# Optimization experiments

Hardware: AMD Instinct MI355X
Metric: run time of the kernel (lower is better)

The kernel has to match this reference:

```python
import jax, jax.numpy as jnp
import numpy as np

H_HEADS = 8
TOP_K = 32


def _interp_matrix(n_out, n_in):
    # 1D linear-interp matrix matching torch trilinear, align_corners=False
    c = (jnp.arange(n_out, dtype=jnp.float32) + 0.5) * (n_in / n_out) - 0.5
    c = jnp.clip(c, 0.0, n_in - 1)
    i0 = jnp.floor(c).astype(jnp.int32)
    i1 = jnp.minimum(i0 + 1, n_in - 1)
    w = c - i0.astype(jnp.float32)
    r = jnp.arange(n_out)
    Mt = jnp.zeros((n_out, n_in), jnp.float32)
    return Mt.at[r, i0].add(1.0 - w).at[r, i1].add(w)


def _ln(x, g, b, eps=1e-5):
    m = x.mean(axis=-1, keepdims=True)
    v = ((x - m) ** 2).mean(axis=-1, keepdims=True)
    return (x - m) * jax.lax.rsqrt(v + eps) * g + b


def _forward(x, mask, pe, Wqkv, bqkv, Wo, bo, ln1_g, ln1_b, W1, b1, W2, b2,
             ln2_g, ln2_b, gate, mem_k, mem_v, fc1_w, fc1_b, fc2_w, fc2_b):
    B, D = x.shape[0], x.shape[1]
    H, HD, K = H_HEADS, D // H_HEADS, TOP_K
    # FeatureConcatenator treated as identity (x already concatenated features)
    Im = _interp_matrix(8, mask.shape[2])  # separable trilinear resize 64->8
    m8 = jnp.einsum('ai,bj,ck,nqijk->nqabc', Im, Im, Im, mask)
    h = x * m8 + pe  # masked features + learned absolute 3D positional enc
    tok = h.reshape(B, D, -1).transpose(0, 2, 1)  # [B, S=512, D]
    scale = 1.0 / jnp.sqrt(jnp.float32(HD))
    L = Wqkv.shape[0]
    for l in range(L):
        qkv = tok @ Wqkv[l] + bqkv[l]
        q, k, v = jnp.split(qkv, 3, axis=-1)
        hd = lambda t: t.reshape(B, -1, H, HD).transpose(0, 2, 1, 3)  # [B,H,S,d]
        q, k, v = hd(q), hd(k), hd(v)
        attn = jax.nn.softmax(jnp.einsum('bhsd,bhtd->bhst', q, k) * scale, axis=-1)
        out = jnp.einsum('bhst,bhtd->bhsd', attn, v)
        if l == 0:  # KNN memory layer: irregular top-k retrieval over memory bank
            sim = jnp.einsum('bhsd,bmd->bhsm', q, mem_k) * scale  # [B,H,S,M]
            top_sim, top_idx = jax.lax.top_k(sim, K)  # [B,H,S,K]
            mv = jnp.take_along_axis(mem_v[:, None, None], top_idx[..., None], axis=3)
            mem_out = jnp.einsum('bhsk,bhskd->bhsd', jax.nn.softmax(top_sim, axis=-1), mv)
            g = jax.nn.sigmoid(gate)[None, :, None, None]
            out = out * (1.0 - g) + mem_out * g
        out = out.transpose(0, 2, 1, 3).reshape(B, -1, D)
        tok = _ln(tok + out @ Wo[l] + bo[l], ln1_g[l], ln1_b[l])
        ff = jax.nn.gelu(tok @ W1[l] + b1[l], approximate=False) @ W2[l] + b2[l]
        tok = _ln(tok + ff, ln2_g[l], ln2_b[l])
    pooled = tok.mean(axis=1)  # global avg pool over all 512 voxels
    return jax.nn.gelu(pooled @ fc1_w + fc1_b, approximate=False) @ fc2_w + fc2_b


def setup_inputs() -> dict:
    key = jax.random.key(0)
    ks = jax.random.split(key, 24)
    B, D, Sp, M, L = 4, 512, 8, 8192, 6
    H, HD, FF, MLP, NC = 8, 64, 2048, 1024, 117
    nrm = lambda k, shp, s=0.02: jax.random.normal(k, shp, jnp.float32) * s
    return {
        'x': jax.random.normal(ks[0], (B, D, Sp, Sp, Sp), jnp.float32),
        'mask': jax.random.uniform(ks[1], (B, 1, 64, 64, 64), jnp.float32),
        'pe': nrm(ks[2], (1, D, Sp, Sp, Sp)),
        'Wqkv': nrm(ks[3], (L, D, 3 * D)),
        'bqkv': jnp.zeros((L, 3 * D), jnp.float32),
        'Wo': nrm(ks[4], (L, D, D)),
        'bo': jnp.zeros((L, D), jnp.float32),
        'ln1_g': jnp.ones((L, D), jnp.float32),
        'ln1_b': jnp.zeros((L, D), jnp.float32),
        'W1': nrm(ks[5], (L, D, FF)),
        'b1': jnp.zeros((L, FF), jnp.float32),
        'W2': nrm(ks[6], (L, FF, D)),
        'b2': jnp.zeros((L, D), jnp.float32),
        'ln2_g': jnp.ones((L, D), jnp.float32),
        'ln2_b': jnp.zeros((L, D), jnp.float32),
        'gate': jnp.zeros((H,), jnp.float32),
        'mem_k': jax.random.normal(ks[7], (B, M, HD), jnp.float32),
        'mem_v': jax.random.normal(ks[8], (B, M, HD), jnp.float32),
        'fc1_w': nrm(ks[9], (D, MLP)),
        'fc1_b': jnp.zeros((MLP,), jnp.float32),
        'fc2_w': nrm(ks[10], (MLP, NC)),
        'fc2_b': jnp.zeros((NC,), jnp.float32),
    }


def reference(x, mask, pe, Wqkv, bqkv, Wo, bo, ln1_g, ln1_b, W1, b1, W2, b2,
              ln2_g, ln2_b, gate, mem_k, mem_v, fc1_w, fc1_b, fc2_w, fc2_b):
    return _forward(x, mask, pe, Wqkv, bqkv, Wo, bo, ln1_g, ln1_b, W1, b1, W2,
                    b2, ln2_g, ln2_b, gate, mem_k, mem_v, fc1_w, fc1_b, fc2_w, fc2_b)
```

## Files before the change

kernel.cpp:

```cpp
#include <hip/hip_runtime.h>
#include <hip/hip_bf16.h>
#include <float.h>
#include <math.h>

#define NB 4
#define ND 512
#define NS 512
#define NH 8
#define NHD 64
#define NM 8192
#define NL 6
#define NFF 2048
#define NMLP 1024
#define NC 117

#define KCC 64
#define NCC (NM / KCC)
#define CAPB 160
#define TRIG 96

#define CAPS 352
#define TRIGS 96

#define AS1 __attribute__((address_space(1)))
// ... 6 lines not shown
    return 0.5f * x * (1.0f + erff(x * 0.70710678118654752440f));
}

__device__ __forceinline__ ushort f2bf_rne(float x) {
    uint u = __float_as_uint(x);
    uint r = u + 0x7FFFu + ((u >> 16) & 1u);
    return (ushort)(r >> 16);
}
__device__ __forceinline__ float bf2f(ushort h) { return __uint_as_float(((uint)h) << 16); }
__device__ __forceinline__ void split1(float x, ushort& h, ushort& l) {
    h = f2bf_rne(x);
    float r = x - bf2f(h);
    l = f2bf_rne(r);
}
__device__ __forceinline__ void split8(const float* v, s16x8& hv, s16x8& lv) {
#pragma unroll
    for (int j = 0; j < 8; ++j) {
        ushort h, l;
        split1(v[j], h, l);
        hv[j] = (short)h;
        lv[j] = (short)l;
    }
}

__device__ __forceinline__ unsigned long long packkey(float v, int idx) {
    uint u = __float_as_uint(v);
    u = u ^ (((int)u < 0) ? 0xFFFFFFFFu : 0x80000000u);
    return (((unsigned long long)u) << 13) | (unsigned long long)(8191 - idx);
}
__device__ __forceinline__ float keyval(unsigned long long K) {
    uint vb = (uint)(K >> 13);
    uint orig = (vb & 0x80000000u) ? (vb ^ 0x80000000u) : ~vb;
    return __uint_as_float(orig);
}

__device__ __forceinline__ void shrink_cheap(float* __restrict__ cval,
                                             ushort* __restrict__ cidx,
                                             int q, int n, int lane,
                                             float* __restrict__ thrOut) {
    if (n < 32) return;
    int j0 = lane, j1 = lane + 64, j2 = lane + 128;
    bool o0 = j0 < n, o1 = j1 < n, o2 = j2 < n;
    float v0 = o0 ? cval[q * CAPB + j0] : 0.f;
    float v1 = o1 ? cval[q * CAPB + j1] : 0.f;
    float v2 = o2 ? cval[q * CAPB + j2] : 0.f;
    ushort i0 = o0 ? cidx[q * CAPB + j0] : 0;
    ushort i1 = o1 ? cidx[q * CAPB + j1] : 0;
    ushort i2 = o2 ? cidx[q * CAPB + j2] : 0;
    unsigned long long k0 = o0 ? packkey(v0, (int)i0) : 0ULL;
    unsigned long long k1 = o1 ? packkey(v1, (int)i1) : 0ULL;
    unsigned long long k2 = o2 ? packkey(v2, (int)i2) : 0ULL;
    unsigned long long lo = 0, hi = (1ULL << 45) - 1;
    while (lo < hi) {
        unsigned long long mid = (lo + hi + 1) >> 1;
        int c = (int)__popcll(__ballot(k0 >= mid)) + (int)__popcll(__ballot(k1 >= mid)) +
                (int)__popcll(__ballot(k2 >= mid));
        if (c >= 32) lo = mid;
        else hi = mid - 1;
    }
    unsigned long long K = lo;
    unsigned long long lm = (1ULL << lane) - 1;
    int base = 0;
    {
        unsigned long long m = __ballot(k0 >= K);
        if (k0 >= K) { int p = base + (int)__popcll(m & lm); cval[q * CAPB + p] = v0; cidx[q * CAPB + p] = i0; }
        base += (int)__popcll(m);
    }
    {
        unsigned long long m = __ballot(k1 >= K);
        if (k1 >= K) { int p = base + (int)__popcll(m & lm); cval[q * CAPB + p] = v1; cidx[q * CAPB + p] = i1; }
        base += (int)__popcll(m);
    }
    {
        unsigned long long m = __ballot(k2 >= K);
        if (k2 >= K) { int p = base + (int)__popcll(m & lm); cval[q * CAPB + p] = v2; cidx[q * CAPB + p] = i2; }
        base += (int)__popcll(m);
    }
    if (thrOut && lane == 0) *thrOut = keyval(K);
}

__device__ __forceinline__ float shrink6b(float* __restrict__ bv,
                                          ushort* __restrict__ bi,
                                          int n, int lane) {
    int j0 = lane, j1 = lane + 64, j2 = lane + 128, j3 = lane + 192, j4 = lane + 256, j5 = lane + 320;
    bool o0 = j0 < n, o1 = j1 < n, o2 = j2 < n, o3 = j3 < n, o4 = j4 < n, o5 = j5 < n;
    float v0 = o0 ? bv[j0] : 0.f, v1 = o1 ? bv[j1] : 0.f, v2 = o2 ? bv[j2] : 0.f;
    float v3 = o3 ? bv[j3] : 0.f, v4 = o4 ? bv[j4] : 0.f, v5 = o5 ? bv[j5] : 0.f;
    ushort i0 = o0 ? bi[j0] : 0, i1 = o1 ? bi[j1] : 0, i2 = o2 ? bi[j2] : 0;
    ushort i3 = o3 ? bi[j3] : 0, i4 = o4 ? bi[j4] : 0, i5 = o5 ? bi[j5] : 0;
    unsigned long long k0 = o0 ? packkey(v0, (int)i0) : 0ULL;
    unsigned long long k1 = o1 ? packkey(v1, (int)i1) : 0ULL;
    unsigned long long k2 = o2 ? packkey(v2, (int)i2) : 0ULL;
    unsigned long long k3 = o3 ? packkey(v3, (int)i3) : 0ULL;
    unsigned long long k4 = o4 ? packkey(v4, (int)i4) : 0ULL;
    unsigned long long k5 = o5 ? packkey(v5, (int)i5) : 0ULL;
    unsigned long long lo = 0, hi = (1ULL << 45) - 1;
    while (lo < hi) {
        unsigned long long mid = (lo + hi + 1) >> 1;
        int c = (int)__popcll(__ballot(k0 >= mid)) + (int)__popcll(__ballot(k1 >= mid)) +
                (int)__popcll(__ballot(k2 >= mid)) + (int)__popcll(__ballot(k3 >= mid)) +
                (int)__popcll(__ballot(k4 >= mid)) + (int)__popcll(__ballot(k5 >= mid));
        if (c >= 32) lo = mid;
        else hi = mid - 1;
    }
    unsigned long long K = lo;
    unsigned long long lm = (1ULL << lane) - 1;
    int base = 0;
    {
        unsigned long long m = __ballot(k0 >= K);
        if (k0 >= K) { int p = base + (int)__popcll(m & lm); bv[p] = v0; bi[p] = i0; }
        base += (int)__popcll(m);
    }
    {
        unsigned long long m = __ballot(k1 >= K);
        if (k1 >= K) { int p = base + (int)__popcll(m & lm); bv[p] = v1; bi[p] = i1; }
        base += (int)__popcll(m);
    }
    {
        unsigned long long m = __ballot(k2 >= K);
        if (k2 >= K) { int p = base + (int)__popcll(m & lm); bv[p] = v2; bi[p] = i2; }
        base += (int)__popcll(m);
    }
    {
        unsigned long long m = __ballot(k3 >= K);
        if (k3 >= K) { int p = base + (int)__popcll(m & lm); bv[p] = v3; bi[p] = i3; }
        base += (int)__popcll(m);
    }
    {
        unsigned long long m = __ballot(k4 >= K);
        if (k4 >= K) { int p = base + (int)__popcll(m & lm); bv[p] = v4; bi[p] = i4; }
        base += (int)__popcll(m);
    }
    {
        unsigned long long m = __ballot(k5 >= K);
        if (k5 >= K) { int p = base + (int)__popcll(m & lm); bv[p] = v5; bi[p] = i5; }
        base += (int)__popcll(m);
    }
    return keyval(K);
}
// ... 132 lines not shown
        int k = ty * 8 + i;
        t[tx][k] = Wl[(size_t)(k0 + k) * N + n0 + tx];
    }
    __syncthreads();
    int tid = ty * 32 + tx;
    int r = tid >> 3, gg = tid & 7;
    float v[8];
#pragma unroll
    for (int j = 0; j < 8; ++j) v[j] = t[r][gg * 8 + j];
    s16x8 hv, lv;
    split8(v, hv, lv);
    size_t byte = (size_t)(n0 + r) * (2 * K) + (size_t)(k0 >> 6) * 128 +
                  (size_t)(((gg * 16)) ^ ((r & 7) << 4));
    *(s16x8*)((char*)WHl + byte) = hv;
    *(s16x8*)((char*)WLl + byte) = lv;
}

__global__ void k_asplit(const float* __restrict__ X, ushort* __restrict__ XH,
                         ushort* __restrict__ XL, int K) {
    int id = blockIdx.x * 256 + threadIdx.x;
    int gtot = K >> 3;
    int m = id / gtot, g = id - m * gtot;
    const float* src = X + (size_t)m * K + g * 8;
    float v[8];
    *(float4*)&v[0] = *(const float4*)(src);
    *(float4*)&v[4] = *(const float4*)(src + 4);
    s16x8 hv, lv;
    split8(v, hv, lv);
    int kc = g >> 3, gg = g & 7;
    size_t byte = (size_t)m * (2 * K) + (size_t)kc * 128 +
                  (size_t)((gg * 16) ^ ((m & 7) << 4));
    *(s16x8*)((char*)XH + byte) = hv;
    *(s16x8*)((char*)XL + byte) = lv;
}

__global__ void k_qkvsplit(const float* __restrict__ qkv, ushort* __restrict__ QH,
                           ushort* __restrict__ QL, ushort* __restrict__ KH,
                           ushort* __restrict__ KL) {
    int id = blockIdx.x * 256 + threadIdx.x;
    int r = id >> 3, g = id & 7;
    int b = r >> 12, h = (r >> 9) & 7, s = r & 511;
    const float* base = qkv + ((size_t)(b * NS + s)) * 1536 + h * 64 + g * 8;
    size_t byte = (size_t)r * 128 + (size_t)((g * 16) ^ ((r & 7) << 4));
    float v[8];
#pragma unroll
    for (int j = 0; j < 8; ++j) v[j] = base[j] * 0.125f;
    s16x8 hv, lv;
    split8(v, hv, lv);
    *(s16x8*)((char*)QH + byte) = hv;
    *(s16x8*)((char*)QL + byte) = lv;
#pragma unroll
    for (int j = 0; j < 8; ++j) v[j] = base[512 + j];
    split8(v, hv, lv);
    *(s16x8*)((char*)KH + byte) = hv;
    *(s16x8*)((char*)KL + byte) = lv;
}

__global__ __launch_bounds__(256) void k_vsplitT(const float* __restrict__ qkv,
                                                 ushort* __restrict__ VTH,
                                                 ushort* __restrict__ VTL) {
    __shared__ float t[64][65];
    int sb = blockIdx.x, h = blockIdx.y, b = blockIdx.z;
    int tid = threadIdx.x;
    {
        int sl = tid >> 2, dseg = (tid & 3) * 16;
        const float* src = qkv + ((size_t)(b * NS) + sb * 64 + sl) * 1536 + 1024 + h * 64 + dseg;
#pragma unroll
        for (int i = 0; i < 4; ++i) {
            float4 v = *(const float4*)(src + i * 4);
            t[sl][dseg + i * 4 + 0] = v.x;
            t[sl][dseg + i * 4 + 1] = v.y;
            t[sl][dseg + i * 4 + 2] = v.z;
            t[sl][dseg + i * 4 + 3] = v.w;
        }
    }
    __syncthreads();
    {
        int dr = tid >> 2, sseg = (tid & 3) * 16;
        size_t rb = ((size_t)(b * NH + h) * 64 + dr) * 1024 + (size_t)sb * 128;
        char* oh = (char*)VTH + rb;
        char* ol = (char*)VTL + rb;
        int sw = (dr & 7) << 4;
#pragma unroll
        for (int i = 0; i < 16; ++i) {
            int s = sseg + i;
            float v = t[s][dr];
            ushort hh, ll;
            split1(v, hh, ll);
            int by = (((s >> 3) * 16) ^ sw) + (s & 7) * 2;
            *(ushort*)(oh + by) = hh;
            *(ushort*)(ol + by) = ll;
        }
    }
}

template <int BM, int BN, int EPI>
__global__ __launch_bounds__(256) void k_gmm(
    const float* __restrict__ A, const float* __restrict__ W,
    const float* __restrict__ bias, const float* __restrict__ resid,
    float* __restrict__ C, int M, int N, int K) {
    constexpr int PAD = 40;
    constexpr int FM = BM / 32, FN = BN / 32;
    __shared__ __align__(16) ushort Ah[BM * PAD];
    __shared__ __align__(16) ushort Al[BM * PAD];
    __shared__ __align__(16) ushort Bh[BN * PAD];
    __shared__ __align__(16) ushort Bl[BN * PAD];
    int tid = threadIdx.x, lane = tid & 63, wvi = tid >> 6;
    int wr = wvi >> 1, wc = wvi & 1;
    int bn = blockIdx.x * BN, bm = blockIdx.y * BM;
    constexpr int FPTA = BM / 8;
    constexpr int TPRA = 32 / FPTA;
    int arow = tid / TPRA;
    int akoff = (tid % TPRA) * FPTA;
    const float* Ap = A + (size_t)(bm + arow) * K + akoff;
    constexpr int FPTB = BN / 8;
    int bkrow = tid >> 3;
    int bnoff = (tid & 7) * FPTB;
    const float* Wp = W + (size_t)bkrow * N + bn + bnoff;
    float abuf[FPTA], bbuf[FPTB];
#pragma unroll
    for (int j = 0; j < FPTA; j += 4) *(float4*)&abuf[j] = *(const float4*)(Ap + j);
#pragma unroll
    for (int j = 0; j < FPTB; j += 4) *(float4*)&bbuf[j] = *(const float4*)(Wp + j);
    f32x4 acc[FM][FN] = {};
    for (int k0 = 0; k0 < K; k0 += 32) {
#pragma unroll
// ... 38 lines not shown
#pragma unroll
            for (int fn = 0; fn < FN; ++fn) {
                acc[fm][fn] = __builtin_amdgcn_mfma_f32_16x16x32_bf16(fah[fm], fbh[fn], acc[fm][fn], 0, 0, 0);
                acc[fm][fn] = __builtin_amdgcn_mfma_f32_16x16x32_bf16(fah[fm], fbl[fn], acc[fm][fn], 0, 0, 0);
                acc[fm][fn] = __builtin_amdgcn_mfma_f32_16x16x32_bf16(fal[fm], fbh[fn], acc[fm][fn], 0, 0, 0);
            }
        __syncthreads();
    }
#pragma unroll
    for (int fm = 0; fm < FM; ++fm) {
#pragma unroll
        for (int fn = 0; fn < FN; ++fn) {
            int n = bn + wc * (BN / 2) + fn * 16 + (lane & 15);
            float bb = 0.f;
            if (EPI != 3) bb = bias[n];
#pragma unroll
            for (int r = 0; r < 4; ++r) {
                int m = bm + wr * (BM / 2) + fm * 16 + (lane >> 4) * 4 + r;
                float o = acc[fm][fn][r] + bb;
                if (EPI == 1) o = gelu_f(o);
                else if (EPI == 2) o += resid[(size_t)m * N + n];
                C[(size_t)m * N + n] = o;
            }
        }
    }
}

template <int BM, int BN, int EPI>
__global__ __launch_bounds__(256) void k_gmm2(
    const ushort* __restrict__ AH, const ushort* __restrict__ AL,
    const ushort* __restrict__ BH, const ushort* __restrict__ BL,
    const float* __restrict__ bias, const float* __restrict__ resid,
    float* __restrict__ C, ushort* __restrict__ CH, ushort* __restrict__ CL,
    int M, int N, int K) {
    constexpr int FM = BM / 32, FN = BN / 32;
    __shared__ __align__(16) ushort sAh[BM * 64];
    __shared__ __align__(16) ushort sAl[BM * 64];
    __shared__ __align__(16) ushort sBh[BN * 64];
    __shared__ __align__(16) ushort sBl[BN * 64];
    int tid = threadIdx.x, lane = tid & 63, wvi = tid >> 6;
    int wr = wvi >> 1, wc = wvi & 1;
    int bn = blockIdx.x * BN, bm = blockIdx.y * BM;
    int rloc = tid >> 3, bgr = (tid & 7) * 16;
    size_t rowstride = (size_t)(2 * K);
    f32x4 acc[FM][FN] = {};

    for (int k0 = 0; k0 < K; k0 += 64) {
        __syncthreads();
        size_t kcb = (size_t)k0 * 2;
#pragma unroll
        for (int i = 0; i < BM / 32; ++i) {
            int r = i * 32 + rloc;
            size_t g = (size_t)(bm + r) * rowstride + kcb + bgr;
            __builtin_amdgcn_global_load_lds((const AS1 uint*)((const char*)AH + g),
                                             (AS3 uint*)((char*)sAh + r * 128 + bgr), 16, 0, 0);
            __builtin_amdgcn_global_load_lds((const AS1 uint*)((const char*)AL + g),
                                             (AS3 uint*)((char*)sAl + r * 128 + bgr), 16, 0, 0);
        }
#pragma unroll
        for (int i = 0; i < BN / 32; ++i) {
            int r = i * 32 + rloc;
            size_t g = (size_t)(bn + r) * rowstride + kcb + bgr;
            __builtin_amdgcn_global_load_lds((const AS1 uint*)((const char*)BH + g),
                                             (AS3 uint*)((char*)sBh + r * 128 + bgr), 16, 0, 0);
            __builtin_amdgcn_global_load_lds((const AS1 uint*)((const char*)BL + g),
                                             (AS3 uint*)((char*)sBl + r * 128 + bgr), 16, 0, 0);
// ... 16 lines not shown
                int by = row * 128 + (kbyte ^ ((row & 7) << 4));
                fbh[fn] = *(const s16x8*)((const char*)sBh + by);
                fbl[fn] = *(const s16x8*)((const char*)sBl + by);
            }
#pragma unroll
            for (int fm = 0; fm < FM; ++fm)
#pragma unroll
                for (int fn = 0; fn < FN; ++fn) {
                    acc[fm][fn] = __builtin_amdgcn_mfma_f32_16x16x32_bf16(fah[fm], fbh[fn], acc[fm][fn], 0, 0, 0);
                    acc[fm][fn] = __builtin_amdgcn_mfma_f32_16x16x32_bf16(fah[fm], fbl[fn], acc[fm][fn], 0, 0, 0);
                    acc[fm][fn] = __builtin_amdgcn_mfma_f32_16x16x32_bf16(fal[fm], fbh[fn], acc[fm][fn], 0, 0, 0);
                }
        }
    }
#pragma unroll
    for (int fm = 0; fm < FM; ++fm) {
#pragma unroll
        for (int fn = 0; fn < FN; ++fn) {
            int n = bn + wc * (BN / 2) + fn * 16 + (lane & 15);
            float bb = 0.f;
            if (EPI != 3) bb = bias[n];
#pragma unroll
            for (int r = 0; r < 4; ++r) {
                int m = bm + wr * (BM / 2) + fm * 16 + (lane >> 4) * 4 + r;
                float o = acc[fm][fn][r] + bb;
                if (EPI == 4) {
                    o = gelu_f(o);
                    ushort hh, ll;
                    split1(o, hh, ll);
                    size_t byb = (size_t)m * 2 * N + (size_t)(n >> 6) * 128 +
                                 (size_t)(((((n >> 3) & 7) * 16)) ^ ((m & 7) << 4)) + (n & 7) * 2;
                    *(ushort*)((char*)CH + byb) = hh;
                    *(ushort*)((char*)CL + byb) = ll;
                } else {
                    if (EPI == 1) o = gelu_f(o);
                    else if (EPI == 2) o += resid[(size_t)m * N + n];
                    C[(size_t)m * N + n] = o;
                }
            }
        }
    }
}

__global__ __launch_bounds__(256) void k_attn2(
    const ushort* __restrict__ QH, const ushort* __restrict__ QL,
    const ushort* __restrict__ KH, const ushort* __restrict__ KL,
    const ushort* __restrict__ VTH, const ushort* __restrict__ VTL,
    float* __restrict__ ao) {
    __shared__ __align__(16) char SM[81920];
    int qt = blockIdx.x, h = blockIdx.y, b = blockIdx.z;
    int tid = threadIdx.x, lane = tid & 63, wvi = tid >> 6;
    size_t R = ((size_t)(b * NH + h)) * NS;
    const char* KHg = (const char*)KH + R * 128;
    const char* KLg = (const char*)KL + R * 128;
    const char* VHg = (const char*)VTH + ((size_t)(b * NH + h) * 64) * 1024;
    const char* VLg = (const char*)VTL + ((size_t)(b * NH + h) * 64) * 1024;

    stage_lin((const char*)QH + (R + qt * 64) * 128, SM + 65536, wvi, lane);
    stage_lin((const char*)QL + (R + qt * 64) * 128, SM + 73728, wvi, lane);
    stage_lin(KHg, SM + 0, wvi, lane);
    stage_lin(KLg, SM + 8192, wvi, lane);
    stage_vt(VHg, 0, SM + 32768, wvi, lane);
    stage_vt(VLg, 0, SM + 40960, wvi, lane);
    __syncthreads();

    s16x8 fqh[2], fql[2];
// ... 188 lines not shown
            int idx = tid + i * 256;
            int r = idx >> 6, d = idx & 63;
            ks[r][d] = base[(size_t)(c * 64 + r) * 1536 + 1024 + h * 64 + d];
        }
        __syncthreads();
#pragma unroll 8
        for (int kk = 0; kk < 64; ++kk) {
            float p0 = sc[ty][kk], p1 = sc[ty + 16][kk];
            float v0 = ks[kk][tx], v1 = ks[kk][tx + 16], v2 = ks[kk][tx + 32], v3 = ks[kk][tx + 48];
            accp[0][0] += p0 * v0; accp[0][1] += p0 * v1; accp[0][2] += p0 * v2; accp[0][3] += p0 * v3;
            accp[1][0] += p1 * v0; accp[1][1] += p1 * v1; accp[1][2] += p1 * v2; accp[1][3] += p1 * v3;
        }
    }
    __syncthreads();
    float inv0 = 1.0f / Srow[ty], inv1 = 1.0f / Srow[ty + 16];
    size_t o0 = ((size_t)(b * NS) + s0 + ty) * ND + h * 64;
    size_t o1 = ((size_t)(b * NS) + s0 + ty + 16) * ND + h * 64;
    ao[o0 + tx] = accp[0][0] * inv0;
    ao[o0 + tx + 16] = accp[0][1] * inv0;
    ao[o0 + tx + 32] = accp[0][2] * inv0;
    ao[o0 + tx + 48] = accp[0][3] * inv0;
    ao[o1 + tx] = accp[1][0] * inv1;
    ao[o1 + tx + 16] = accp[1][1] * inv1;
    ao[o1 + tx + 32] = accp[1][2] * inv1;
    ao[o1 + tx + 48] = accp[1][3] * inv1;
}

__global__ __launch_bounds__(256) void k_ksel(
    const float* __restrict__ sims, const float* __restrict__ mv,
    const float* __restrict__ gate, float* __restrict__ ao, int b) {
    __shared__ float bval[4][CAPS];
    __shared__ ushort bidx[4][CAPS];
    int tid = threadIdx.x, lane = tid & 63, wvi = tid >> 6;
    int q = blockIdx.x * 4 + wvi;
    const float* srow = sims + (size_t)q * NM;
    float* bv = &bval[wvi][0];
    ushort* bi = &bidx[wvi][0];
    unsigned long long lm = (1ULL << lane) - 1;
    {
        float4 v = *(const float4*)(srow + lane * 4);
        int m0 = lane * 4;
        bv[m0 + 0] = v.x; bi[m0 + 0] = (ushort)(m0 + 0);
        bv[m0 + 1] = v.y; bi[m0 + 1] = (ushort)(m0 + 1);
        bv[m0 + 2] = v.z; bi[m0 + 2] = (ushort)(m0 + 2);
        bv[m0 + 3] = v.w; bi[m0 + 3] = (ushort)(m0 + 3);
    }
    float thr = shrink6b(bv, bi, 256, lane);
    int cnt = 32;
    float4 vcur = *(const float4*)(srow + 256 + lane * 4);
    for (int i = 1; i < 32; ++i) {
        float4 vnext;
        if (i + 1 < 32) vnext = *(const float4*)(srow + (size_t)(i + 1) * 256 + lane * 4);
        int m0 = i * 256 + lane * 4;
        bool px = vcur.x >= thr, py = vcur.y >= thr, pz = vcur.z >= thr, pw = vcur.w >= thr;
        unsigned long long bx = __ballot(px), by = __ballot(py), bz = __ballot(pz), bw = __ballot(pw);
        int nx = (int)__popcll(bx), ny = (int)__popcll(by), nz = (int)__popcll(bz), nw = (int)__popcll(bw);
        int b0 = cnt, b1 = b0 + nx, b2 = b1 + ny, b3 = b2 + nz;
        if (px) { int p = b0 + (int)__popcll(bx & lm); bv[p] = vcur.x; bi[p] = (ushort)(m0 + 0); }
        if (py) { int p = b1 + (int)__popcll(by & lm); bv[p] = vcur.y; bi[p] = (ushort)(m0 + 1); }
        if (pz) { int p = b2 + (int)__popcll(bz & lm); bv[p] = vcur.z; bi[p] = (ushort)(m0 + 2); }
        if (pw) { int p = b3 + (int)__popcll(bw & lm); bv[p] = vcur.w; bi[p] = (ushort)(m0 + 3); }
        cnt = b3 + nw;
        if (cnt >= TRIGS) {
            thr = shrink6b(bv, bi, cnt, lane);
            cnt = 32;
        }
        vcur = vnext;
    }
    thr = shrink6b(bv, bi, cnt, lane);
    float val = (lane < 32) ? bv[lane] : -FLT_MAX;
    float mx = val;
#pragma unroll
    for (int off = 32; off; off >>= 1) mx = fmaxf(mx, __shfl_xor(mx, off));
    float e = (lane < 32) ? __expf(val - mx) : 0.f;
    float ssum = e;
#pragma unroll
    for (int off = 32; off; off >>= 1) ssum += __shfl_xor(ssum, off);
    float w = e / ssum;
    if (lane < 32) bv[lane] = w;
    float acc = 0.f;
    const float* vb = mv + (size_t)b * NM * NHD;
#pragma unroll 4
    for (int j = 0; j < 32; ++j) {
        float ww = bv[j];
        int idx = (int)bi[j];
        acc += ww * vb[(size_t)idx * NHD + lane];
    }
    int h = q >> 9, s = q & 511;
    float g = 1.0f / (1.0f + __expf(-gate[h]));
    float* aop = ao + ((size_t)(b * NS) + s) * ND + h * 64 + lane;
    *aop = *aop * (1.0f - g) + acc * g;
}

__global__ __launch_bounds__(256, 2) void k_knn5(
    const float* __restrict__ qkv, const ushort* __restrict__ mkh,
    const ushort* __restrict__ mkl, const float* __restrict__ mv,
    const float* __restrict__ gate, float* __restrict__ ao) {
    __shared__ __align__(16) char SM[63760];
    ushort* kh0 = (ushort*)SM;
    ushort* kl0 = (ushort*)(SM + 8192);
    ushort* kh1 = (ushort*)(SM + 16384);
    ushort* kl1 = (ushort*)(SM + 24576);
    float* cval = (float*)(SM + 32768);
    ushort* cidx = (ushort*)(SM + 53248);
    float* thrV = (float*)(SM + 63488);
    int* cnt = (int*)(SM + 63616);
    int* sflag = (int*)(SM + 63744);
    ushort* qh = (ushort*)(SM + 32768);
    ushort* ql = (ushort*)(SM + 36864);
    int b = blockIdx.y, s0 = blockIdx.x * 4;
    int tid = threadIdx.x, lane = tid & 63, wvi = tid >> 6;
    const ushort* mhb = mkh + (size_t)b * NM * 64;
    const ushort* mlb = mkl + (size_t)b * NM * 64;
    {
        int q = tid >> 3, dbase = (tid & 7) * 8;
        const float* src = &qkv[((size_t)(b * NS) + s0 + (q & 3)) * 1536 + (q >> 2) * 64 + dbase];
        float v[8];
#pragma unroll
        for (int j = 0; j < 8; ++j) v[j] = src[j] * 0.125f;
        s16x8 hv, lv;
        split8(v, hv, lv);
        int by = q * 128 + ((dbase * 2) ^ ((q & 7) << 4));
        *(s16x8*)((char*)qh + by) = hv;
        *(s16x8*)((char*)ql + by) = lv;
// ... 231 lines not shown
    const float* b2   = (const float*)d_in[12];
    const float* ln2g = (const float*)d_in[13];
    const float* ln2b = (const float*)d_in[14];
    const float* gate = (const float*)d_in[15];
    const float* memk = (const float*)d_in[16];
    const float* memv = (const float*)d_in[17];
    const float* fc1w = (const float*)d_in[18];
    const float* fc1b = (const float*)d_in[19];
    const float* fc2w = (const float*)d_in[20];
    const float* fc2b = (const float*)d_in[21];
    float* out = (float*)d_out;

    float* ws = (float*)d_ws;

    float* m8     = ws;
    ushort* mkh   = (ushort*)(m8 + 2048);
    ushort* mkl   = mkh + 2097152;
    float* tok    = (float*)(mkl + 2097152);
    float* qkv    = tok + 1048576;
    float* ao     = qkv + 3145728;
    float* pooled = ao + 1048576;
    float* o1     = pooled + 2048;
    ushort* aH    = (ushort*)(o1 + 4096);
    ushort* aL    = aH + 1048576;
    ushort* WqTH  = aL + 1048576;
    ushort* WqTL  = WqTH + 4718592;
    ushort* WoTH  = WqTL + 4718592;
    ushort* WoTL  = WoTH + 1572864;
    ushort* W1TH  = WoTL + 1572864;
    ushort* W1TL  = W1TH + 6291456;
    ushort* W2TH  = W1TL + 6291456;
    ushort* W2TL  = W2TH + 6291456;
    float* simsb  = (float*)(W2TL + 6291456);
    float* ff1  = simsb;
    ushort* fH  = (ushort*)(simsb + 4194304);
    ushort* fL  = fH + 4194304;
    float* ybuf = simsb + 8388608;
    ushort* KHb  = (ushort*)(simsb + 9437184);
    ushort* KLb  = KHb + 1048576;
    ushort* VTHb = KLb + 1048576;
    ushort* VTLb = VTHb + 1048576;
    (void)ff1;

    size_t needNew = (size_t)((simsb + 33554432) - ws) * sizeof(float);

    if (ws_size >= needNew) {
        k_m8<<<NB, 512, 0, stream>>>(mask, m8);
        k_mksplit<<<1024, 256, 0, stream>>>(memk, mkh, mkl);
        k_tok<<<dim3(16, 16, NB), dim3(32, 8), 0, stream>>>(x, pe, m8, tok);
        k_wsplitT<<<dim3(48, 8, 6), dim3(32, 8), 0, stream>>>(Wqkv, WqTH, WqTL, 512, 1536);
        k_wsplitT<<<dim3(16, 8, 6), dim3(32, 8), 0, stream>>>(Wo, WoTH, WoTL, 512, 512);
        k_wsplitT<<<dim3(64, 8, 6), dim3(32, 8), 0, stream>>>(W1, W1TH, W1TL, 512, 2048);
        k_wsplitT<<<dim3(16, 32, 6), dim3(32, 8), 0, stream>>>(W2, W2TH, W2TL, 2048, 512);
        k_asplit<<<512, 256, 0, stream>>>(tok, aH, aL, 512);

        for (int l = 0; l < NL; ++l) {
            k_gmm2<128, 128, 0><<<dim3(12, 16), 256, 0, stream>>>(
                aH, aL, WqTH + (size_t)l * 786432, WqTL + (size_t)l * 786432,
                bqkv + l * 1536, nullptr, qkv, nullptr, nullptr, 2048, 1536, 512);
            k_qkvsplit<<<512, 256, 0, stream>>>(qkv, aH, aL, KHb, KLb);
            k_vsplitT<<<dim3(8, NH, NB), 256, 0, stream>>>(qkv, VTHb, VTLb);
            k_attn2<<<dim3(8, NH, NB), 256, 0, stream>>>(aH, aL, KHb, KLb, VTHb, VTLb, ao);
            if (l == 0) {
                for (int bb = 0; bb < NB; ++bb) {
                    k_gmm2<128, 128, 3><<<dim3(64, 32), 256, 0, stream>>>(
                        aH + (size_t)bb * 262144, aL + (size_t)bb * 262144,
                        mkh + (size_t)bb * 524288, mkl + (size_t)bb * 524288,
                        nullptr, nullptr, simsb, nullptr, nullptr, 4096, 8192, 64);
                    k_ksel<<<1024, 256, 0, stream>>>(simsb, memv, gate, ao, bb);
                }
            }
            k_asplit<<<512, 256, 0, stream>>>(ao, aH, aL, 512);
            k_gmm2<64, 64, 2><<<dim3(8, 32), 256, 0, stream>>>(
                aH, aL, WoTH + (size_t)l * 262144, WoTL + (size_t)l * 262144,
                bo + l * 512, tok, ybuf, nullptr, nullptr, 2048, 512, 512);
            k_ln2<<<2048, 256, 0, stream>>>(ybuf, ln1g + l * 512, ln1b + l * 512, tok, aH, aL);
            k_gmm2<128, 128, 4><<<dim3(16, 16), 256, 0, stream>>>(
                aH, aL, W1TH + (size_t)l * 1048576, W1TL + (size_t)l * 1048576,
                b1 + l * 2048, nullptr, nullptr, fH, fL, 2048, 2048, 512);
            k_gmm2<64, 64, 2><<<dim3(8, 32), 256, 0, stream>>>(
                fH, fL, W2TH + (size_t)l * 1048576, W2TL + (size_t)l * 1048576,
                b2 + l * 512, tok, ybuf, nullptr, nullptr, 2048, 512, 2048);
            k_ln2<<<2048, 256, 0, stream>>>(ybuf, ln2g + l * 512, ln2b + l * 512, tok, aH, aL);
        }
        k_pool<<<NB, 512, 0, stream>>>(tok, pooled);
        k_fc1<<<16, 256, 0, stream>>>(pooled, fc1w, fc1b, o1);
        k_fc2<<<2, 256, 0, stream>>>(o1, fc2w, fc2b, out);
        return;
    }

    float* m8b     = ws;
    ushort* mkh2   = (ushort*)(m8b + 2048);
    ushort* mkl2   = mkh2 + 2097152;
    float* tok2    = (float*)(mkl2 + 2097152);
    float* qkv2    = tok2 + 1048576;
    float* ao2     = qkv2 + 3145728;
    float* ybuf2   = ao2 + 1048576;
    float* ff12    = ybuf2 + 1048576;
    float* pooled2 = ff12 + 4194304;
    float* o12     = pooled2 + 2048;
    float* qmat2   = o12 + 4096;
    float* memkT2  = qmat2 + 1048576;
    float* simsb2  = memkT2 + 2097152;

    size_t needMid = (size_t)((simsb2 + 33554432) - ws) * sizeof(float);
    bool big = ws_size >= needMid;

    k_m8<<<NB, 512, 0, stream>>>(mask, m8b);
    if (big)
        k_memkT<<<dim3(NM / 32, 2, NB), dim3(32, 8), 0, stream>>>(memk, memkT2);
    else
        k_mksplit<<<1024, 256, 0, stream>>>(memk, mkh2, mkl2);
    k_tok<<<dim3(16, 16, NB), dim3(32, 8), 0, stream>>>(x, pe, m8b, tok2);

    for (int l = 0; l < NL; ++l) {
        k_gmm<128, 128, 0><<<dim3(12, 16), 256, 0, stream>>>(
            tok2, Wqkv + (size_t)l * 512 * 1536, bqkv + l * 1536, nullptr, qkv2, 2048, 1536, 512);
        k_attn<<<dim3(16, NH, NB), 256, 0, stream>>>(qkv2, ao2);
        if (l == 0) {
            if (big) {
                k_qmat<<<1024, 256, 0, stream>>>(qkv2, qmat2);
                for (int bb = 0; bb < NB; ++bb) {
                    k_gmm<128, 128, 3><<<dim3(64, 32), 256, 0, stream>>>(
                        qmat2 + (size_t)bb * 262144, memkT2 + (size_t)bb * 524288,
                        nullptr, nullptr, simsb2, 4096, 8192, 64);
                    k_ksel<<<1024, 256, 0, stream>>>(simsb2, memv, gate, ao2, bb);
                }
            } else {
                k_knn5<<<dim3(NS / 4, NB), 256, 0, stream>>>(qkv2, mkh2, mkl2, memv, gate, ao2);
            }
        }
        k_gmm<64, 64, 2><<<dim3(8, 32), 256, 0, stream>>>(
            ao2, Wo + (size_t)l * 512 * 512, bo + l * 512, tok2, ybuf2, 2048, 512, 512);
        k_ln<<<2048, 256, 0, stream>>>(ybuf2, ln1g + l * 512, ln1b + l * 512, tok2);
        k_gmm<128, 128, 1><<<dim3(16, 16), 256, 0, stream>>>(
            tok2, W1 + (size_t)l * 512 * 2048, b1 + l * 2048, nullptr, ff12, 2048, 2048, 512);
        k_gmm<64, 64, 2><<<dim3(8, 32), 256, 0, stream>>>(
            ff12, W2 + (size_t)l * 2048 * 512, b2 + l * 512, tok2, ybuf2, 2048, 512, 2048);
        k_ln<<<2048, 256, 0, stream>>>(ybuf2, ln2g + l * 512, ln2b + l * 512, tok2);
    }
    k_pool<<<NB, 512, 0, stream>>>(tok2, pooled2);
    k_fc1<<<16, 256, 0, stream>>>(pooled2, fc1w, fc1b, o12);
    k_fc2<<<2, 256, 0, stream>>>(o12, fc2w, fc2b, out);
}
```

Before: 1.435 ms.

## Fuse QKV split into GEMM epilogue and parallelize top-k selection across half-rows

The QKV GEMM now writes the hi/lo bf16-split Q (pre-scaled), K and transposed V directly in the swizzled layouts attention expects, which removes the separate qkvsplit and vsplitT kernels and the fp32 qkv round trip. The top-k selection kernel now splits each similarity row across two wavefronts that each scan half the memory bank, then merges the two candidate sets, so twice as many blocks are launched. The threshold search becomes a 32-bit radix bit search on the value with a tie fallback to the 45-bit packed key. The GEMM epilogue now uses scattered 2-byte stores, and the merge adds a block barrier.

```diff
diff --git a/kernel.cpp b/kernel.cpp
--- a/kernel.cpp
+++ b/kernel.cpp
@@ -62,6 +62,14 @@
     uint vb = (uint)(K >> 13);
     uint orig = (vb & 0x80000000u) ? (vb ^ 0x80000000u) : ~vb;
     return __uint_as_float(orig);
+}
+__device__ __forceinline__ uint sortable32(float v) {
+    uint u = __float_as_uint(v);
+    return u ^ (((int)u < 0) ? 0xFFFFFFFFu : 0x80000000u);
+}
+__device__ __forceinline__ float unsortable32(uint s) {
+    uint u = (s & 0x80000000u) ? (s ^ 0x80000000u) : ~s;
+    return __uint_as_float(u);
 }
 
 __device__ __forceinline__ void shrink_cheap(float* __restrict__ cval,
@@ -109,7 +117,7 @@
     if (thrOut && lane == 0) *thrOut = keyval(K);
 }
 
-__device__ __forceinline__ float shrink6b(float* __restrict__ bv,
+__device__ __forceinline__ float shrink6v(float* __restrict__ bv,
                                           ushort* __restrict__ bi,
                                           int n, int lane) {
     int j0 = lane, j1 = lane + 64, j2 = lane + 128, j3 = lane + 192, j4 = lane + 256, j5 = lane + 320;
@@ -118,23 +126,58 @@
     float v3 = o3 ? bv[j3] : 0.f, v4 = o4 ? bv[j4] : 0.f, v5 = o5 ? bv[j5] : 0.f;
     ushort i0 = o0 ? bi[j0] : 0, i1 = o1 ? bi[j1] : 0, i2 = o2 ? bi[j2] : 0;
     ushort i3 = o3 ? bi[j3] : 0, i4 = o4 ? bi[j4] : 0, i5 = o5 ? bi[j5] : 0;
+    uint s0 = o0 ? sortable32(v0) : 0u, s1 = o1 ? sortable32(v1) : 0u;
+    uint s2 = o2 ? sortable32(v2) : 0u, s3 = o3 ? sortable32(v3) : 0u;
+    uint s4 = o4 ? sortable32(v4) : 0u, s5 = o5 ? sortable32(v5) : 0u;
+    uint S = 0;
+#pragma unroll 1
+    for (int bit = 31; bit >= 0; --bit) {
+        uint cand = S | (1u << bit);
+        int c = (int)__popcll(__ballot(s0 >= cand)) + (int)__popcll(__ballot(s1 >= cand)) +
+                (int)__popcll(__ballot(s2 >= cand)) + (int)__popcll(__ballot(s3 >= cand)) +
+                (int)__popcll(__ballot(s4 >= cand)) + (int)__popcll(__ballot(s5 >= cand));
+        if (c >= 32) S = cand;
+    }
+    unsigned long long g0 = __ballot(s0 > S), g1 = __ballot(s1 > S), g2 = __ballot(s2 > S);
+    unsigned long long g3 = __ballot(s3 > S), g4 = __ballot(s4 > S), g5 = __ballot(s5 > S);
+    unsigned long long e0 = __ballot(o0 && s0 == S), e1 = __ballot(o1 && s1 == S), e2 = __ballot(o2 && s2 == S);
+    unsigned long long e3 = __ballot(o3 && s3 == S), e4 = __ballot(o4 && s4 == S), e5 = __ballot(o5 && s5 == S);
+    int cgt = (int)__popcll(g0) + (int)__popcll(g1) + (int)__popcll(g2) +
+              (int)__popcll(g3) + (int)__popcll(g4) + (int)__popcll(g5);
+    int ceq = (int)__popcll(e0) + (int)__popcll(e1) + (int)__popcll(e2) +
+              (int)__popcll(e3) + (int)__popcll(e4) + (int)__popcll(e5);
+    unsigned long long lm = (1ULL << lane) - 1;
+    if (cgt + ceq == 32) {
+        int base = 0;
+        if (s0 > S) { int p = base + (int)__popcll(g0 & lm); bv[p] = v0; bi[p] = i0; } base += (int)__popcll(g0);
+        if (s1 > S) { int p = base + (int)__popcll(g1 & lm); bv[p] = v1; bi[p] = i1; } base += (int)__popcll(g1);
+        if (s2 > S) { int p = base + (int)__popcll(g2 & lm); bv[p] = v2; bi[p] = i2; } base += (int)__popcll(g2);
+        if (s3 > S) { int p = base + (int)__popcll(g3 & lm); bv[p] = v3; bi[p] = i3; } base += (int)__popcll(g3);
+        if (s4 > S) { int p = base + (int)__popcll(g4 & lm); bv[p] = v4; bi[p] = i4; } base += (int)__popcll(g4);
+        if (s5 > S) { int p = base + (int)__popcll(g5 & lm); bv[p] = v5; bi[p] = i5; } base += (int)__popcll(g5);
+        if (o0 && s0 == S) { int p = base + (int)__popcll(e0 & lm); bv[p] = v0; bi[p] = i0; } base += (int)__popcll(e0);
+        if (o1 && s1 == S) { int p = base + (int)__popcll(e1 & lm); bv[p] = v1; bi[p] = i1; } base += (int)__popcll(e1);
+        if (o2 && s2 == S) { int p = base + (int)__popcll(e2 & lm); bv[p] = v2; bi[p] = i2; } base += (int)__popcll(e2);
+        if (o3 && s3 == S) { int p = base + (int)__popcll(e3 & lm); bv[p] = v3; bi[p] = i3; } base += (int)__popcll(e3);
+        if (o4 && s4 == S) { int p = base + (int)__popcll(e4 & lm); bv[p] = v4; bi[p] = i4; } base += (int)__popcll(e4);
+        if (o5 && s5 == S) { int p = base + (int)__popcll(e5 & lm); bv[p] = v5; bi[p] = i5; }
+        return unsortable32(S);
+    }
     unsigned long long k0 = o0 ? packkey(v0, (int)i0) : 0ULL;
     unsigned long long k1 = o1 ? packkey(v1, (int)i1) : 0ULL;
     unsigned long long k2 = o2 ? packkey(v2, (int)i2) : 0ULL;
     unsigned long long k3 = o3 ? packkey(v3, (int)i3) : 0ULL;
     unsigned long long k4 = o4 ? packkey(v4, (int)i4) : 0ULL;
     unsigned long long k5 = o5 ? packkey(v5, (int)i5) : 0ULL;
-    unsigned long long lo = 0, hi = (1ULL << 45) - 1;
-    while (lo < hi) {
-        unsigned long long mid = (lo + hi + 1) >> 1;
-        int c = (int)__popcll(__ballot(k0 >= mid)) + (int)__popcll(__ballot(k1 >= mid)) +
-                (int)__popcll(__ballot(k2 >= mid)) + (int)__popcll(__ballot(k3 >= mid)) +
-                (int)__popcll(__ballot(k4 >= mid)) + (int)__popcll(__ballot(k5 >= mid));
-        if (c >= 32) lo = mid;
-        else hi = mid - 1;
-    }
-    unsigned long long K = lo;
-    unsigned long long lm = (1ULL << lane) - 1;
+    unsigned long long K = 0;
+#pragma unroll 1
+    for (int bit = 44; bit >= 0; --bit) {
+        unsigned long long cand = K | (1ULL << bit);
+        int c = (int)__popcll(__ballot(k0 >= cand)) + (int)__popcll(__ballot(k1 >= cand)) +
+                (int)__popcll(__ballot(k2 >= cand)) + (int)__popcll(__ballot(k3 >= cand)) +
+                (int)__popcll(__ballot(k4 >= cand)) + (int)__popcll(__ballot(k5 >= cand));
+        if (c >= 32) K = cand;
+    }
     int base = 0;
     {
         unsigned long long m = __ballot(k0 >= K);
@@ -333,66 +376,6 @@
                   (size_t)((gg * 16) ^ ((m & 7) << 4));
     *(s16x8*)((char*)XH + byte) = hv;
     *(s16x8*)((char*)XL + byte) = lv;
-}
-
-__global__ void k_qkvsplit(const float* __restrict__ qkv, ushort* __restrict__ QH,
-                           ushort* __restrict__ QL, ushort* __restrict__ KH,
-                           ushort* __restrict__ KL) {
-    int id = blockIdx.x * 256 + threadIdx.x;
-    int r = id >> 3, g = id & 7;
-    int b = r >> 12, h = (r >> 9) & 7, s = r & 511;
-    const float* base = qkv + ((size_t)(b * NS + s)) * 1536 + h * 64 + g * 8;
-    size_t byte = (size_t)r * 128 + (size_t)((g * 16) ^ ((r & 7) << 4));
-    float v[8];
-#pragma unroll
-    for (int j = 0; j < 8; ++j) v[j] = base[j] * 0.125f;
-    s16x8 hv, lv;
-    split8(v, hv, lv);
-    *(s16x8*)((char*)QH + byte) = hv;
-    *(s16x8*)((char*)QL + byte) = lv;
-#pragma unroll
-    for (int j = 0; j < 8; ++j) v[j] = base[512 + j];
-    split8(v, hv, lv);
-    *(s16x8*)((char*)KH + byte) = hv;
-    *(s16x8*)((char*)KL + byte) = lv;
-}
-
-__global__ __launch_bounds__(256) void k_vsplitT(const float* __restrict__ qkv,
-                                                 ushort* __restrict__ VTH,
-                                                 ushort* __restrict__ VTL) {
-    __shared__ float t[64][65];
-    int sb = blockIdx.x, h = blockIdx.y, b = blockIdx.z;
-    int tid = threadIdx.x;
-    {
-        int sl = tid >> 2, dseg = (tid & 3) * 16;
-        const float* src = qkv + ((size_t)(b * NS) + sb * 64 + sl) * 1536 + 1024 + h * 64 + dseg;
-#pragma unroll
-        for (int i = 0; i < 4; ++i) {
-            float4 v = *(const float4*)(src + i * 4);
-            t[sl][dseg + i * 4 + 0] = v.x;
-            t[sl][dseg + i * 4 + 1] = v.y;
-            t[sl][dseg + i * 4 + 2] = v.z;
-            t[sl][dseg + i * 4 + 3] = v.w;
-        }
-    }
-    __syncthreads();
-    {
-        int dr = tid >> 2, sseg = (tid & 3) * 16;
-        size_t rb = ((size_t)(b * NH + h) * 64 + dr) * 1024 + (size_t)sb * 128;
-        char* oh = (char*)VTH + rb;
-        char* ol = (char*)VTL + rb;
-        int sw = (dr & 7) << 4;
-#pragma unroll
-        for (int i = 0; i < 16; ++i) {
-            int s = sseg + i;
-            float v = t[s][dr];
-            ushort hh, ll;
-            split1(v, hh, ll);
-            int by = (((s >> 3) * 16) ^ sw) + (s & 7) * 2;
-            *(ushort*)(oh + by) = hh;
-            *(ushort*)(ol + by) = ll;
-        }
-    }
 }
 
 template <int BM, int BN, int EPI>
@@ -497,6 +480,8 @@
     const ushort* __restrict__ BH, const ushort* __restrict__ BL,
     const float* __restrict__ bias, const float* __restrict__ resid,
     float* __restrict__ C, ushort* __restrict__ CH, ushort* __restrict__ CL,
+    ushort* __restrict__ C2H, ushort* __restrict__ C2L,
+    ushort* __restrict__ C3H, ushort* __restrict__ C3L,
     int M, int N, int K) {
     constexpr int FM = BM / 32, FN = BN / 32;
     __shared__ __align__(16) ushort sAh[BM * 64];
@@ -579,6 +564,31 @@
                                  (size_t)(((((n >> 3) & 7) * 16)) ^ ((m & 7) << 4)) + (n & 7) * 2;
                     *(ushort*)((char*)CH + byb) = hh;
                     *(ushort*)((char*)CL + byb) = ll;
+                } else if (EPI == 5) {
+                    int seg = n >> 9;
+                    int hh_ = (n >> 6) & 7, dd = n & 63;
+                    int bq = m >> 9, sq = m & 511;
+                    ushort hh, ll;
+                    if (seg == 0) {
+                        split1(o * 0.125f, hh, ll);
+                        size_t rr = (size_t)bq * 4096 + hh_ * 512 + sq;
+                        size_t by = rr * 128 + (size_t)((((dd >> 3) * 16)) ^ ((sq & 7) << 4)) + (dd & 7) * 2;
+                        *(ushort*)((char*)CH + by) = hh;
+                        *(ushort*)((char*)CL + by) = ll;
+                    } else if (seg == 1) {
+                        split1(o, hh, ll);
+                        size_t rr = (size_t)bq * 4096 + hh_ * 512 + sq;
+                        size_t by = rr * 128 + (size_t)((((dd >> 3) * 16)) ^ ((sq & 7) << 4)) + (dd & 7) * 2;
+                        *(ushort*)((char*)C2H + by) = hh;
+                        *(ushort*)((char*)C2L + by) = ll;
+                    } else {
+                        split1(o, hh, ll);
+                        size_t rr = (size_t)(bq * 8 + hh_) * 64 + dd;
+                        size_t by = rr * 1024 + (size_t)(sq >> 6) * 128 +
+                                    (size_t)(((((sq >> 3) & 7) * 16)) ^ ((dd & 7) << 4)) + (sq & 7) * 2;
+                        *(ushort*)((char*)C3H + by) = hh;
+                        *(ushort*)((char*)C3L + by) = ll;
+                    }
                 } else {
                     if (EPI == 1) o = gelu_f(o);
                     else if (EPI == 2) o += resid[(size_t)m * N + n];
@@ -833,64 +843,91 @@
     __shared__ float bval[4][CAPS];
     __shared__ ushort bidx[4][CAPS];
     int tid = threadIdx.x, lane = tid & 63, wvi = tid >> 6;
-    int q = blockIdx.x * 4 + wvi;
-    const float* srow = sims + (size_t)q * NM;
+    int q = blockIdx.x * 2 + (wvi >> 1);
+    int hf = wvi & 1;
+    const float* sr = sims + (size_t)q * NM + hf * 4096;
     float* bv = &bval[wvi][0];
     ushort* bi = &bidx[wvi][0];
     unsigned long long lm = (1ULL << lane) - 1;
+
     {
-        float4 v = *(const float4*)(srow + lane * 4);
+        float4 v = *(const float4*)(sr + lane * 4);
         int m0 = lane * 4;
-        bv[m0 + 0] = v.x; bi[m0 + 0] = (ushort)(m0 + 0);
-        bv[m0 + 1] = v.y; bi[m0 + 1] = (ushort)(m0 + 1);
-        bv[m0 + 2] = v.z; bi[m0 + 2] = (ushort)(m0 + 2);
-        bv[m0 + 3] = v.w; bi[m0 + 3] = (ushort)(m0 + 3);
-    }
-    float thr = shrink6b(bv, bi, 256, lane);
+        int gI = hf * 4096 + m0;
+        bv[m0 + 0] = v.x; bi[m0 + 0] = (ushort)(gI + 0);
+        bv[m0 + 1] = v.y; bi[m0 + 1] = (ushort)(gI + 1);
+        bv[m0 + 2] = v.z; bi[m0 + 2] = (ushort)(gI + 2);
+        bv[m0 + 3] = v.w; bi[m0 + 3] = (ushort)(gI + 3);
+    }
+    float thr = shrink6v(bv, bi, 256, lane);
     int cnt = 32;
-    float4 vcur = *(const float4*)(srow + 256 + lane * 4);
-    for (int i = 1; i < 32; ++i) {
-        float4 vnext;
-        if (i + 1 < 32) vnext = *(const float4*)(srow + (size_t)(i + 1) * 256 + lane * 4);
-        int m0 = i * 256 + lane * 4;
-        bool px = vcur.x >= thr, py = vcur.y >= thr, pz = vcur.z >= thr, pw = vcur.w >= thr;
+
+    float4 vA = *(const float4*)(sr + 256 + lane * 4);
+    float4 vB = *(const float4*)(sr + 512 + lane * 4);
+    for (int i = 1; i < 16; ++i) {
+        float4 vC = vB;
+        if (i + 2 < 16) vC = *(const float4*)(sr + (size_t)(i + 2) * 256 + lane * 4);
+        int m0 = hf * 4096 + i * 256 + lane * 4;
+        bool px = vA.x >= thr, py = vA.y >= thr, pz = vA.z >= thr, pw = vA.w >= thr;
         unsigned long long bx = __ballot(px), by = __ballot(py), bz = __ballot(pz), bw = __ballot(pw);
         int nx = (int)__popcll(bx), ny = (int)__popcll(by), nz = (int)__popcll(bz), nw = (int)__popcll(bw);
         int b0 = cnt, b1 = b0 + nx, b2 = b1 + ny, b3 = b2 + nz;
-        if (px) { int p = b0 + (int)__popcll(bx & lm); bv[p] = vcur.x; bi[p] = (ushort)(m0 + 0); }
-        if (py) { int p = b1 + (int)__popcll(by & lm); bv[p] = vcur.y; bi[p] = (ushort)(m0 + 1); }
-        if (pz) { int p = b2 + (int)__popcll(bz & lm); bv[p] = vcur.z; bi[p] = (ushort)(m0 + 2); }
-        if (pw) { int p = b3 + (int)__popcll(bw & lm); bv[p] = vcur.w; bi[p] = (ushort)(m0 + 3); }
+        if (px) { int p = b0 + (int)__popcll(bx & lm); bv[p] = vA.x; bi[p] = (ushort)(m0 + 0); }
+        if (py) { int p = b1 + (int)__popcll(by & lm); bv[p] = vA.y; bi[p] = (ushort)(m0 + 1); }
+        if (pz) { int p = b2 + (int)__popcll(bz & lm); bv[p] = vA.z; bi[p] = (ushort)(m0 + 2); }
+        if (pw) { int p = b3 + (int)__popcll(bw & lm); bv[p] = vA.w; bi[p] = (ushort)(m0 + 3); }
         cnt = b3 + nw;
         if (cnt >= TRIGS) {
-            thr = shrink6b(bv, bi, cnt, lane);
+            thr = shrink6v(bv, bi, cnt, lane);
             cnt = 32;
         }
-        vcur = vnext;
-    }
-    thr = shrink6b(bv, bi, cnt, lane);
-    float val = (lane < 32) ? bv[lane] : -FLT_MAX;
-    float mx = val;
-#pragma unroll
-    for (int off = 32; off; off >>= 1) mx = fmaxf(mx, __shfl_xor(mx, off));
-    float e = (lane < 32) ? __expf(val - mx) : 0.f;
-    float ssum = e;
-#pragma unroll
-    for (int off = 32; off; off >>= 1) ssum += __shfl_xor(ssum, off);
-    float w = e / ssum;
-    if (lane < 32) bv[lane] = w;
-    float acc = 0.f;
-    const float* vb = mv + (size_t)b * NM * NHD;
+        vA = vB;
+        vB = vC;
+    }
+    thr = shrink6v(bv, bi, cnt, lane);
+    __syncthreads();
+
+    if (hf == 0) {
+        float mval;
+        ushort midx;
+        if (lane < 32) { mval = bval[wvi][lane]; midx = bidx[wvi][lane]; }
+        else { mval = bval[wvi + 1][lane - 32]; midx = bidx[wvi + 1][lane - 32]; }
+        unsigned long long k = packkey(mval, (int)midx);
+        unsigned long long K = 0;
+#pragma unroll 1
+        for (int bit = 44; bit >= 0; --bit) {
+            unsigned long long cand = K | (1ULL << bit);
+            if ((int)__popcll(__ballot(k >= cand)) >= 32) K = cand;
+        }
+        unsigned long long m = __ballot(k >= K);
+        if (k >= K) {
+            int p = (int)__popcll(m & lm);
+            bv[p] = mval;
+            bi[p] = midx;
+        }
+        float val = (lane < 32) ? bv[lane] : -FLT_MAX;
+        float mx = val;
+#pragma unroll
+        for (int off = 32; off; off >>= 1) mx = fmaxf(mx, __shfl_xor(mx, off));
+        float e = (lane < 32) ? __expf(val - mx) : 0.f;
+        float ssum = e;
+#pragma unroll
+        for (int off = 32; off; off >>= 1) ssum += __shfl_xor(ssum, off);
+        float w = e / ssum;
+        if (lane < 32) bv[lane] = w;
+        float acc = 0.f;
+        const float* vb = mv + (size_t)b * NM * NHD;
 #pragma unroll 4
-    for (int j = 0; j < 32; ++j) {
-        float ww = bv[j];
-        int idx = (int)bi[j];
-        acc += ww * vb[(size_t)idx * NHD + lane];
-    }
-    int h = q >> 9, s = q & 511;
-    float g = 1.0f / (1.0f + __expf(-gate[h]));
-    float* aop = ao + ((size_t)(b * NS) + s) * ND + h * 64 + lane;
-    *aop = *aop * (1.0f - g) + acc * g;
+        for (int j = 0; j < 32; ++j) {
+            float ww = bv[j];
+            int idx = (int)bi[j];
+            acc += ww * vb[(size_t)idx * NHD + lane];
+        }
+        int h = q >> 9, s = q & 511;
+        float g = 1.0f / (1.0f + __expf(-gate[h]));
+        float* aop = ao + ((size_t)(b * NS) + s) * ND + h * 64 + lane;
+        *aop = *aop * (1.0f - g) + acc * g;
+    }
 }
 
 __global__ __launch_bounds__(256, 2) void k_knn5(
@@ -1188,15 +1225,15 @@
     ushort* W2TH  = W1TL + 6291456;
     ushort* W2TL  = W2TH + 6291456;
     float* simsb  = (float*)(W2TL + 6291456);
-    float* ff1  = simsb;
     ushort* fH  = (ushort*)(simsb + 4194304);
     ushort* fL  = fH + 4194304;
     float* ybuf = simsb + 8388608;
-    ushort* KHb  = (ushort*)(simsb + 9437184);
+    ushort* QHb  = (ushort*)qkv;
+    ushort* QLb  = QHb + 1048576;
+    ushort* KHb  = QLb + 1048576;
     ushort* KLb  = KHb + 1048576;
     ushort* VTHb = KLb + 1048576;
     ushort* VTLb = VTHb + 1048576;
-    (void)ff1;
 
     size_t needNew = (size_t)((simsb + 33554432) - ws) * sizeof(float);
 
@@ -1211,32 +1248,35 @@
         k_asplit<<<512, 256, 0, stream>>>(tok, aH, aL, 512);
 
         for (int l = 0; l < NL; ++l) {
-            k_gmm2<128, 128, 0><<<dim3(12, 16), 256, 0, stream>>>(
+            k_gmm2<128, 128, 5><<<dim3(12, 16), 256, 0, stream>>>(
                 aH, aL, WqTH + (size_t)l * 786432, WqTL + (size_t)l * 786432,
-                bqkv + l * 1536, nullptr, qkv, nullptr, nullptr, 2048, 1536, 512);
-            k_qkvsplit<<<512, 256, 0, stream>>>(qkv, aH, aL, KHb, KLb);
-            k_vsplitT<<<dim3(8, NH, NB), 256, 0, stream>>>(qkv, VTHb, VTLb);
-            k_attn2<<<dim3(8, NH, NB), 256, 0, stream>>>(aH, aL, KHb, KLb, VTHb, VTLb, ao);
+                bqkv + l * 1536, nullptr, nullptr, QHb, QLb, KHb, KLb, VTHb, VTLb,
+                2048, 1536, 512);
+            k_attn2<<<dim3(8, NH, NB), 256, 0, stream>>>(QHb, QLb, KHb, KLb, VTHb, VTLb, ao);
             if (l == 0) {
                 for (int bb = 0; bb < NB; ++bb) {
                     k_gmm2<128, 128, 3><<<dim3(64, 32), 256, 0, stream>>>(
-                        aH + (size_t)bb * 262144, aL + (size_t)bb * 262144,
+                        QHb + (size_t)bb * 262144, QLb + (size_t)bb * 262144,
                         mkh + (size_t)bb * 524288, mkl + (size_t)bb * 524288,
-                        nullptr, nullptr, simsb, nullptr, nullptr, 4096, 8192, 64);
-                    k_ksel<<<1024, 256, 0, stream>>>(simsb, memv, gate, ao, bb);
+                        nullptr, nullptr, simsb, nullptr, nullptr, nullptr, nullptr,
+                        nullptr, nullptr, 4096, 8192, 64);
+                    k_ksel<<<2048, 256, 0, stream>>>(simsb, memv, gate, ao, bb);
                 }
             }
             k_asplit<<<512, 256, 0, stream>>>(ao, aH, aL, 512);
             k_gmm2<64, 64, 2><<<dim3(8, 32), 256, 0, stream>>>(
                 aH, aL, WoTH + (size_t)l * 262144, WoTL + (size_t)l * 262144,
-                bo + l * 512, tok, ybuf, nullptr, nullptr, 2048, 512, 512);
+                bo + l * 512, tok, ybuf, nullptr, nullptr, nullptr, nullptr,
+                nullptr, nullptr, 2048, 512, 512);
             k_ln2<<<2048, 256, 0, stream>>>(ybuf, ln1g + l * 512, ln1b + l * 512, tok, aH, aL);
             k_gmm2<128, 128, 4><<<dim3(16, 16), 256, 0, stream>>>(
                 aH, aL, W1TH + (size_t)l * 1048576, W1TL + (size_t)l * 1048576,
-                b1 + l * 2048, nullptr, nullptr, fH, fL, 2048, 2048, 512);
+                b1 + l * 2048, nullptr, nullptr, fH, fL, nullptr, nullptr,
+                nullptr, nullptr, 2048, 2048, 512);
             k_gmm2<64, 64, 2><<<dim3(8, 32), 256, 0, stream>>>(
                 fH, fL, W2TH + (size_t)l * 1048576, W2TL + (size_t)l * 1048576,
-                b2 + l * 512, tok, ybuf, nullptr, nullptr, 2048, 512, 2048);
+                b2 + l * 512, tok, ybuf, nullptr, nullptr, nullptr, nullptr,
+                nullptr, nullptr, 2048, 512, 2048);
             k_ln2<<<2048, 256, 0, stream>>>(ybuf, ln2g + l * 512, ln2b + l * 512, tok, aH, aL);
         }
         k_pool<<<NB, 512, 0, stream>>>(tok, pooled);
@@ -1280,7 +1320,7 @@
                     k_gmm<128, 128, 3><<<dim3(64, 32), 256, 0, stream>>>(
                         qmat2 + (size_t)bb * 262144, memkT2 + (size_t)bb * 524288,
                         nullptr, nullptr, simsb2, 4096, 8192, 64);
-                    k_ksel<<<1024, 256, 0, stream>>>(simsb2, memv, gate, ao2, bb);
+                    k_ksel<<<2048, 256, 0, stream>>>(simsb2, memv, gate, ao2, bb);
                 }
             } else {
                 k_knn5<<<dim3(NS / 4, NB), 256, 0, stream>>>(qkv2, mkh2, mkl2, memv, gate, ao2);
```

Result: faster. 1.392 ms (-3.0%).
